# Performance work log

Measured on AMD Instinct MI355X. Metric: run time of the kernel, lower is better.

## Reference

```python
import jax, jax.numpy as jnp
import numpy as np

ROPE_BASE = 100.0  # CroCo/InfiniteVGGT-style 2D RoPE base

def _rope_1d(sub, pos, base=ROPE_BASE):
    # sub: (B,H,N,half), pos: (B,N) float
    half = sub.shape[-1]
    quarter = half // 2
    inv_freq = 1.0 / (base ** (jnp.arange(quarter, dtype=jnp.float32) / quarter))
    ang = pos[:, None, :, None] * inv_freq  # (B,1,N,quarter)
    cos, sin = jnp.cos(ang), jnp.sin(ang)
    x1, x2 = sub[..., :quarter], sub[..., quarter:]
    return jnp.concatenate([x1 * cos - x2 * sin, x1 * sin + x2 * cos], axis=-1)

def rope_2d(t, positions):
    # t: (B,H,N,Dh); positions: (B,N,2) int (y,x)
    Dh = t.shape[-1]
    half = Dh // 2
    pos_f = positions.astype(t.dtype)
    y = _rope_1d(t[..., :half], pos_f[..., 0])
    x = _rope_1d(t[..., half:], pos_f[..., 1])
    return jnp.concatenate([y, x], axis=-1)

def setup_inputs() -> dict:
    key = jax.random.key(0)
    k1, k2, k3, k4 = jax.random.split(key, 4)
    B, N, C, H = 2, 2048, 1024, 16
    x = jax.random.normal(k1, (B, N, C), dtype=jnp.float32)
    positions = jax.random.randint(k2, (B, N, 2), 0, 64, dtype=jnp.int32)
    qkv_w = jax.random.normal(k3, (3 * C, C), dtype=jnp.float32) * (C ** -0.5)
    proj_w = jax.random.normal(k4, (C, C), dtype=jnp.float32) * (C ** -0.5)
    proj_b = jnp.zeros((C,), dtype=jnp.float32)
    return {"x": x, "positions": positions, "qkv_w": qkv_w, "proj_w": proj_w, "proj_b": proj_b}

def reference(x, positions, qkv_w, proj_w, proj_b):
    B, N, C = x.shape
    H = 16
    Dh = C // H
    scale = Dh ** -0.5
    qkv = (x @ qkv_w.T).reshape(B, N, 3, H, Dh).transpose(2, 0, 3, 1, 4)  # (3,B,H,N,Dh)
    q, k, v = qkv[0], qkv[1], qkv[2]
    q = rope_2d(q, positions)
    k = rope_2d(k, positions)
    attn = jnp.einsum('bhnd,bhmd->bhnm', q, k) * scale  # (B,H,N,N)
    attn = jax.nn.softmax(attn, axis=-1)
    out = jnp.einsum('bhnm,bhmd->bhnd', attn, v)  # (B,H,N,Dh)
    out = out.transpose(0, 2, 1, 3).reshape(B, N, C)
    return out @ proj_w.T + proj_b
```

## Files before the change

kernel.cpp:

```cpp
#include <hip/hip_runtime.h>
#include <cmath>

typedef unsigned short u16;
typedef unsigned int   u32;
typedef __attribute__((ext_vector_type(8))) __bf16 bf16x8;
typedef __attribute__((ext_vector_type(2))) __bf16 bf16x2;
typedef __attribute__((ext_vector_type(4))) float  f32x4;

constexpr int BB = 2, SEQ = 2048, CH = 1024, NH = 16, DH = 64;

__device__ inline u16 f2bf(float f) {
    u32 u = __builtin_bit_cast(u32, f);
    u += 0x7FFF + ((u >> 16) & 1);
    return (u16)(u >> 16);
}
__device__ inline float bf2f(u16 b) { return __builtin_bit_cast(float, (u32)b << 16); }
__device__ inline u32 pkbf(float a, float b) {
#if __has_builtin(__builtin_amdgcn_cvt_pk_bf16_f32)
    bf16x2 r = __builtin_amdgcn_cvt_pk_bf16_f32(a, b);
    return __builtin_bit_cast(u32, r);
#else
    return (u32)f2bf(a) | ((u32)f2bf(b) << 16);
#endif
}
__device__ inline float fexp2(float x) {
#if __has_builtin(__builtin_amdgcn_exp2f)
    return __builtin_amdgcn_exp2f(x);
#else
    return exp2f(x);
#endif
}

__device__ inline void gld_lds16(const void* g, void* l) {
    __builtin_amdgcn_global_load_lds((const __attribute__((address_space(1))) void*)g,
                                     (__attribute__((address_space(3))) void*)l, 16, 0, 0);
}
__device__ inline f32x4 mfma16(bf16x8 a, bf16x8 b, f32x4 c) {
    return __builtin_amdgcn_mfma_f32_16x16x32_bf16(a, b, c, 0, 0, 0);
}
__device__ inline bf16x8 ld_frag(const u16* p) {
    return __builtin_bit_cast(bf16x8, *(const uint4*)p);
}

__global__ __launch_bounds__(256) void convert_kernel(const float* __restrict__ x,
                                                      const float* __restrict__ wq,
                                                      const float* __restrict__ wp,
                                                      u16* __restrict__ xb,
                                                      u16* __restrict__ wqb,
                                                      u16* __restrict__ wpb) {
    const int q = blockIdx.x * 256 + threadIdx.x;
    const float* src; u16* dst; int idx;
    if (q < 1048576)            { src = x;  dst = xb;  idx = q; }
    else if (q < 1048576+786432){ src = wq; dst = wqb; idx = q - 1048576; }
    else                        { src = wp; dst = wpb; idx = q - 1048576 - 786432; }
    float4 v = *(const float4*)(src + (size_t)idx * 4);
    ushort4 o; o.x = f2bf(v.x); o.y = f2bf(v.y); o.z = f2bf(v.z); o.w = f2bf(v.w);
    *(ushort4*)(dst + (size_t)idx * 4) = o;
}

__global__ __launch_bounds__(256) void gemm_qkv_rope(const u16* __restrict__ A,
                                                     const u16* __restrict__ Bw,
                                                     const int* __restrict__ pos,
                                                     u16* __restrict__ Qb,
                                                     u16* __restrict__ Kb,
                                                     u16* __restrict__ Vt) {
    __shared__ u16 smem[18432];
    u16* As = smem;
    u16* Bs = smem + 4096;
    const int t = threadIdx.x, lane = t & 63, w = t >> 6;
    const int l15 = lane & 15, quad = lane >> 4;
    const int wm = w >> 1, wn = w & 1;
    const int m0 = blockIdx.y * 128, n0 = blockIdx.x * 128;
    const int K = CH, N = 3 * CH;

    const int row0 = t >> 2, v0 = t & 3;
    const int gi0 = (v0 - (row0 >> 1)) & 3;
    const int row1 = row0 + 64;
    const int gi1 = (v0 - (row1 >> 1)) & 3;

    f32x4 acc[4][4] = {};
    for (int k0 = 0; k0 < K; k0 += 32) {
        __syncthreads();
        gld_lds16(A  + (size_t)(m0 + row0) * K + k0 + gi0 * 8, As + t * 8);
        gld_lds16(A  + (size_t)(m0 + row1) * K + k0 + gi1 * 8, As + 2048 + t * 8);
        gld_lds16(Bw + (size_t)(n0 + row0) * K + k0 + gi0 * 8, Bs + t * 8);
        gld_lds16(Bw + (size_t)(n0 + row1) * K + k0 + gi1 * 8, Bs + 2048 + t * 8);
        __syncthreads();
        bf16x8 af[4], bfv[4];
#pragma unroll
        for (int mi = 0; mi < 4; ++mi) {
            const int r = wm * 64 + mi * 16 + l15;
            af[mi] = ld_frag(As + (r * 4 + ((quad + (r >> 1)) & 3)) * 8);
        }
#pragma unroll
        for (int nj = 0; nj < 4; ++nj) {
            const int r = wn * 64 + nj * 16 + l15;
            bfv[nj] = ld_frag(Bs + (r * 4 + ((quad + (r >> 1)) & 3)) * 8);
        }
#pragma unroll
        for (int mi = 0; mi < 4; ++mi)
#pragma unroll
            for (int nj = 0; nj < 4; ++nj)
                acc[mi][nj] = mfma16(af[mi], bfv[nj], acc[mi][nj]);
    }

    const int reg = n0 >> 10;
    const int h   = ((n0 & 1023) >> 6) + wn;
    if (reg < 2) {
        const float fr = exp2f(-(float)l15 * 0.41524101186092f);
        const float scale = reg ? 1.0f : 0.18033688011112042f;
        u16* dst = reg ? Kb : Qb;
#pragma unroll
        for (int mi = 0; mi < 4; ++mi) {
#pragma unroll
            for (int r = 0; r < 4; ++r) {
                const int m = m0 + wm * 64 + mi * 16 + quad * 4 + r;
                const int bh = (m >> 11) * NH + h;
                const int n  = m & 2047;
                float sy, cy, sx, cx;
                sincosf((float)pos[m * 2]     * fr, &sy, &cy);
                sincosf((float)pos[m * 2 + 1] * fr, &sx, &cx);
                cy *= scale; sy *= scale; cx *= scale; sx *= scale;
                const float x1 = acc[mi][0][r], x2 = acc[mi][1][r];
                const float y1 = acc[mi][2][r], y2 = acc[mi][3][r];
                u16* p = dst + ((size_t)bh * SEQ + n) * 64 + l15;
                p[0]  = f2bf(x1 * cy - x2 * sy);
                p[16] = f2bf(x1 * sy + x2 * cy);
                p[32] = f2bf(y1 * cx - y2 * sx);
                p[48] = f2bf(y1 * sx + y2 * cx);
            }
        }
    } else {
        __syncthreads();
        u16* T = smem + w * 4608;
#pragma unroll
        for (int mi = 0; mi < 4; ++mi)
#pragma unroll
            for (int nj = 0; nj < 4; ++nj)
#pragma unroll
                for (int r = 0; r < 4; ++r)
                    T[(nj * 16 + l15) * 72 + mi * 16 + quad * 4 + r] =
                        f2bf(acc[mi][nj][r]);
        const int bh = (m0 >> 11) * NH + h;
        const int nbase = (m0 & 2047) + wm * 64;
        u16* gdst = Vt + ((size_t)bh * 64 + lane) * SEQ + nbase;
#pragma unroll
        for (int j = 0; j < 8; ++j)
            *(uint4*)(gdst + j * 8) = *(const uint4*)(T + lane * 72 + j * 8);
    }
}

__global__ __launch_bounds__(256) void gemm_bf16(const u16* __restrict__ A,
                                                 const u16* __restrict__ Bw,
                                                 const float* __restrict__ bias,
                                                 float* __restrict__ C,
                                                 int M, int N, int K) {
    __shared__ u16 As[128 * 32];
    __shared__ u16 Bs[128 * 32];
    const int t = threadIdx.x, lane = t & 63, w = t >> 6;
    const int l15 = lane & 15, quad = lane >> 4;
    const int wm = w >> 1, wn = w & 1;
    const int m0 = blockIdx.y * 128, n0 = blockIdx.x * 128;

    const int row0 = t >> 2, v0 = t & 3;
    const int gi0 = (v0 - (row0 >> 1)) & 3;
    const int row1 = row0 + 64;
    const int gi1 = (v0 - (row1 >> 1)) & 3;

    f32x4 acc[4][4] = {};
    for (int k0 = 0; k0 < K; k0 += 32) {
        __syncthreads();
        gld_lds16(A  + (size_t)(m0 + row0) * K + k0 + gi0 * 8, As + t * 8);
        gld_lds16(A  + (size_t)(m0 + row1) * K + k0 + gi1 * 8, As + 2048 + t * 8);
        gld_lds16(Bw + (size_t)(n0 + row0) * K + k0 + gi0 * 8, Bs + t * 8);
        gld_lds16(Bw + (size_t)(n0 + row1) * K + k0 + gi1 * 8, Bs + 2048 + t * 8);
        __syncthreads();
        bf16x8 af[4], bfv[4];
#pragma unroll
        for (int mi = 0; mi < 4; ++mi) {
            const int r = wm * 64 + mi * 16 + l15;
            af[mi] = ld_frag(As + (r * 4 + ((quad + (r >> 1)) & 3)) * 8);
        }
#pragma unroll
        for (int nj = 0; nj < 4; ++nj) {
            const int r = wn * 64 + nj * 16 + l15;
            bfv[nj] = ld_frag(Bs + (r * 4 + ((quad + (r >> 1)) & 3)) * 8);
        }
#pragma unroll
        for (int mi = 0; mi < 4; ++mi)
#pragma unroll
            for (int nj = 0; nj < 4; ++nj)
                acc[mi][nj] = mfma16(af[mi], bfv[nj], acc[mi][nj]);
    }
#pragma unroll
    for (int mi = 0; mi < 4; ++mi)
#pragma unroll
        for (int nj = 0; nj < 4; ++nj) {
            const int n = n0 + wn * 64 + nj * 16 + l15;
            const float bv = bias[n];
#pragma unroll
            for (int r = 0; r < 4; ++r) {
                const int m = m0 + wm * 64 + mi * 16 + quad * 4 + r;
                C[(size_t)m * N + n] = acc[mi][nj][r] + bv;
            }
        }
}

__global__ __launch_bounds__(256, 4) void attn_mfma(const u16* __restrict__ Qb,
                                                    const u16* __restrict__ Kb,
                                                    const u16* __restrict__ Vt,
                                                    u16* __restrict__ Opart,
                                                    float* __restrict__ lpart) {
    __shared__ u16 Ks[64 * 64];
    __shared__ u16 Vs[64 * 64];
    __shared__ u16 Ps[128 * 72];
    const int t = threadIdx.x, lane = t & 63, w = t >> 6;
    const int l15 = lane & 15, quad = lane >> 4;
    const int bh = blockIdx.y;
    const int q0 = blockIdx.x * 128;
    const int z  = blockIdx.z;

    const int rowA = t >> 3, vA = t & 7;
    const int giA = (vA - rowA) & 7;
    const int rowB = rowA + 32;
    const int giB = (vA - rowB) & 7;

    const size_t kbase = (size_t)bh * SEQ * 64;
    const size_t vbase = (size_t)bh * 64 * SEQ;

    const uint4 ones_u = {0x3F803F80u, 0x3F803F80u, 0x3F803F80u, 0x3F803F80u};
    const bf16x8 onesf = __builtin_bit_cast(bf16x8, ones_u);

    bf16x8 aq[2][2];
#pragma unroll
    for (int mi = 0; mi < 2; ++mi)
#pragma unroll
        for (int ks = 0; ks < 2; ++ks)
            aq[mi][ks] = ld_frag(Qb + ((size_t)bh * SEQ + q0 + w * 32 + mi * 16 + l15) * 64
                                 + ks * 32 + quad * 8);

    f32x4 oacc[2][4] = {};
    f32x4 lacc[2] = {};

    for (int kt = 0; kt < 16; ++kt) {
        const int k0 = z * 1024 + kt * 64;
        __syncthreads();
        gld_lds16(Kb + kbase + (size_t)(k0 + rowA) * 64 + giA * 8, Ks + t * 8);
        gld_lds16(Kb + kbase + (size_t)(k0 + rowB) * 64 + giB * 8, Ks + 2048 + t * 8);
        gld_lds16(Vt + vbase + (size_t)rowA * SEQ + k0 + giA * 8, Vs + t * 8);
        gld_lds16(Vt + vbase + (size_t)rowB * SEQ + k0 + giB * 8, Vs + 2048 + t * 8);
        __syncthreads();

        f32x4 sacc[2][4] = {};
#pragma unroll
        for (int ks = 0; ks < 2; ++ks)
#pragma unroll
            for (int nk = 0; nk < 4; ++nk) {
                const int rK = nk * 16 + l15;
                const bf16x8 kf = ld_frag(Ks + (rK * 8 + (((ks * 4 + quad) + rK) & 7)) * 8);
                sacc[0][nk] = mfma16(kf, aq[0][ks], sacc[0][nk]);
                sacc[1][nk] = mfma16(kf, aq[1][ks], sacc[1][nk]);
            }

#pragma unroll
        for (int mi = 0; mi < 2; ++mi) {
            const int prow = (w * 32 + mi * 16 + l15) * 72;
#pragma unroll
            for (int nk = 0; nk < 4; ++nk) {
                const float p0 = fexp2(sacc[mi][nk][0]);
                const float p1 = fexp2(sacc[mi][nk][1]);
                const float p2 = fexp2(sacc[mi][nk][2]);
                const float p3 = fexp2(sacc[mi][nk][3]);
                uint2 pk; pk.x = pkbf(p0, p1); pk.y = pkbf(p2, p3);
                *(uint2*)&Ps[prow + nk * 16 + quad * 4] = pk;
            }
        }

#pragma unroll
        for (int ks = 0; ks < 2; ++ks) {
            const bf16x8 ap0 = ld_frag(Ps + (w * 32 + l15) * 72 + ks * 32 + quad * 8);
            const bf16x8 ap1 = ld_frag(Ps + (w * 32 + 16 + l15) * 72 + ks * 32 + quad * 8);
            lacc[0] = mfma16(ap0, onesf, lacc[0]);
            lacc[1] = mfma16(ap1, onesf, lacc[1]);
#pragma unroll
            for (int nj = 0; nj < 4; ++nj) {
                const int rV = nj * 16 + l15;
                const bf16x8 vf = ld_frag(Vs + (rV * 8 + (((ks * 4 + quad) + rV) & 7)) * 8);
                oacc[0][nj] = mfma16(ap0, vf, oacc[0][nj]);
                oacc[1][nj] = mfma16(ap1, vf, oacc[1][nj]);
            }
        }
    }

#pragma unroll
    for (int mi = 0; mi < 2; ++mi)
#pragma unroll
        for (int r = 0; r < 4; ++r) {
            const int qrow = q0 + w * 32 + mi * 16 + quad * 4 + r;
            if (l15 == 0)
                lpart[((size_t)z * 32 + bh) * SEQ + qrow] = lacc[mi][r];
            const size_t orow = (((size_t)z * 32 + bh) * SEQ + qrow) * 64;
#pragma unroll
            for (int nj = 0; nj < 4; ++nj)
                Opart[orow + nj * 16 + l15] = f2bf(oacc[mi][nj][r]);
        }
}

__global__ __launch_bounds__(256) void merge_kernel(const u16* __restrict__ Opart,
                                                    const float* __restrict__ lpart,
                                                    u16* __restrict__ Ob) {
    const int gid = blockIdx.x * 256 + threadIdx.x;
    const int d4 = gid & 15, q = (gid >> 4) & 2047, bh = gid >> 15;
    const size_t i1 = ((size_t)bh * SEQ + q) * 64 + d4 * 4;
    const size_t i2 = i1 + (size_t)32 * SEQ * 64;
    const float inv = 1.0f / (lpart[(size_t)bh * SEQ + q] +
                              lpart[(size_t)(32 + bh) * SEQ + q]);
    const ushort4 a = *(const ushort4*)(Opart + i1);
    const ushort4 b = *(const ushort4*)(Opart + i2);
    ushort4 o;
    o.x = f2bf((bf2f(a.x) + bf2f(b.x)) * inv);
    o.y = f2bf((bf2f(a.y) + bf2f(b.y)) * inv);
    o.z = f2bf((bf2f(a.z) + bf2f(b.z)) * inv);
    o.w = f2bf((bf2f(a.w) + bf2f(b.w)) * inv);
    const int b_ = bh >> 4, h = bh & 15;
    *(ushort4*)(Ob + ((size_t)(b_ * SEQ + q)) * CH + h * 64 + d4 * 4) = o;
}

extern "C" void kernel_launch(void* const* d_in, const int* in_sizes, int n_in,
                              void* d_out, int out_size, void* d_ws, size_t ws_size,
                              hipStream_t stream) {
    const float* x      = (const float*)d_in[0];
    const int*   pos    = (const int*)d_in[1];
    const float* qkv_w  = (const float*)d_in[2];
    const float* proj_w = (const float*)d_in[3];
    const float* proj_b = (const float*)d_in[4];
    float* out = (float*)d_out;

    u16* ws = (u16*)d_ws;
    u16* x_bf    = ws;
    u16* attn_bf = ws;
    u16* wq_bf   = ws + 4194304;
    float* lpart = (float*)(ws + 4194304);
    u16* wp_bf   = ws + 7340032;
    u16* Qb      = ws + 8388608;
    u16* Kb      = ws + 12582912;
    u16* Vt      = ws + 16777216;
    u16* Opart   = ws + 20971520;

    const int M = BB * SEQ;

    convert_kernel<<<8192, 256, 0, stream>>>(x, qkv_w, proj_w, x_bf, wq_bf, wp_bf);
    gemm_qkv_rope<<<dim3(3 * CH / 128, M / 128), 256, 0, stream>>>(
        x_bf, wq_bf, pos, Qb, Kb, Vt);
    attn_mfma<<<dim3(SEQ / 128, BB * NH, 2), 256, 0, stream>>>(Qb, Kb, Vt, Opart, lpart);
    merge_kernel<<<4096, 256, 0, stream>>>(Opart, lpart, attn_bf);
    gemm_bf16<<<dim3(CH / 128, M / 128), 256, 0, stream>>>(
        attn_bf, wp_bf, proj_b, out, M, CH, CH);
}
```

Measured before the change: 218.3 us.

## Double-buffer LDS in both GEMMs and precompute RoPE sin/cos table

Both GEMM kernels now prefetch the next K-tile into a second LDS buffer while computing on the current one, cutting one barrier per iteration and overlapping global loads with MFMA. The convert kernel additionally builds a small cos/sin table (with the Q scale folded in) so the QKV epilogue does table lookups instead of sincosf. The table assumes positions are below 64 and is placed in a workspace region later reused by attention partials.

```diff
diff --git a/kernel.cpp b/kernel.cpp
--- a/kernel.cpp
+++ b/kernel.cpp
@@ -47,8 +47,23 @@
                                                       const float* __restrict__ wp,
                                                       u16* __restrict__ xb,
                                                       u16* __restrict__ wqb,
-                                                      u16* __restrict__ wpb) {
+                                                      u16* __restrict__ wpb,
+                                                      float2* __restrict__ tabq,
+                                                      float2* __restrict__ tabk) {
     const int q = blockIdx.x * 256 + threadIdx.x;
+    if (q >= 2097152) {
+        const int idx = q - 2097152;
+        if (idx < 1024) {
+            const int p = idx >> 4, i = idx & 15;
+            const float f = exp2f(-(float)i * 0.41524101186092f);
+            float s, c;
+            sincosf((float)p * f, &s, &c);
+            tabk[idx] = make_float2(c, s);
+            tabq[idx] = make_float2(c * 0.18033688011112042f,
+                                    s * 0.18033688011112042f);
+        }
+        return;
+    }
     const float* src; u16* dst; int idx;
     if (q < 1048576)            { src = x;  dst = xb;  idx = q; }
     else if (q < 1048576+786432){ src = wq; dst = wqb; idx = q - 1048576; }
@@ -61,41 +76,57 @@
 __global__ __launch_bounds__(256) void gemm_qkv_rope(const u16* __restrict__ A,
                                                      const u16* __restrict__ Bw,
                                                      const int* __restrict__ pos,
+                                                     const float2* __restrict__ tabq,
+                                                     const float2* __restrict__ tabk,
                                                      u16* __restrict__ Qb,
                                                      u16* __restrict__ Kb,
                                                      u16* __restrict__ Vt) {
     __shared__ u16 smem[18432];
-    u16* As = smem;
-    u16* Bs = smem + 4096;
     const int t = threadIdx.x, lane = t & 63, w = t >> 6;
     const int l15 = lane & 15, quad = lane >> 4;
     const int wm = w >> 1, wn = w & 1;
     const int m0 = blockIdx.y * 128, n0 = blockIdx.x * 128;
-    const int K = CH, N = 3 * CH;
+    const int K = CH;
 
     const int row0 = t >> 2, v0 = t & 3;
     const int gi0 = (v0 - (row0 >> 1)) & 3;
     const int row1 = row0 + 64;
     const int gi1 = (v0 - (row1 >> 1)) & 3;
 
+    const u16* A0 = A  + (size_t)(m0 + row0) * K + gi0 * 8;
+    const u16* A1 = A  + (size_t)(m0 + row1) * K + gi1 * 8;
+    const u16* B0 = Bw + (size_t)(n0 + row0) * K + gi0 * 8;
+    const u16* B1 = Bw + (size_t)(n0 + row1) * K + gi1 * 8;
+
+    gld_lds16(A0, smem + t * 8);
+    gld_lds16(A1, smem + 2048 + t * 8);
+    gld_lds16(B0, smem + 8192 + t * 8);
+    gld_lds16(B1, smem + 10240 + t * 8);
+
     f32x4 acc[4][4] = {};
-    for (int k0 = 0; k0 < K; k0 += 32) {
+    for (int kt = 0; kt < K / 32; ++kt) {
         __syncthreads();
-        gld_lds16(A  + (size_t)(m0 + row0) * K + k0 + gi0 * 8, As + t * 8);
-        gld_lds16(A  + (size_t)(m0 + row1) * K + k0 + gi1 * 8, As + 2048 + t * 8);
-        gld_lds16(Bw + (size_t)(n0 + row0) * K + k0 + gi0 * 8, Bs + t * 8);
-        gld_lds16(Bw + (size_t)(n0 + row1) * K + k0 + gi1 * 8, Bs + 2048 + t * 8);
-        __syncthreads();
+        const int cur = (kt & 1) * 4096;
+        if (kt + 1 < K / 32) {
+            const int off = (kt + 1) * 32;
+            const int nxt = ((kt + 1) & 1) * 4096;
+            gld_lds16(A0 + off, smem + nxt + t * 8);
+            gld_lds16(A1 + off, smem + nxt + 2048 + t * 8);
+            gld_lds16(B0 + off, smem + 8192 + nxt + t * 8);
+            gld_lds16(B1 + off, smem + 8192 + nxt + 2048 + t * 8);
+        }
+        const u16* as = smem + cur;
+        const u16* bs = smem + 8192 + cur;
         bf16x8 af[4], bfv[4];
 #pragma unroll
         for (int mi = 0; mi < 4; ++mi) {
             const int r = wm * 64 + mi * 16 + l15;
-            af[mi] = ld_frag(As + (r * 4 + ((quad + (r >> 1)) & 3)) * 8);
+            af[mi] = ld_frag(as + (r * 4 + ((quad + (r >> 1)) & 3)) * 8);
         }
 #pragma unroll
         for (int nj = 0; nj < 4; ++nj) {
             const int r = wn * 64 + nj * 16 + l15;
-            bfv[nj] = ld_frag(Bs + (r * 4 + ((quad + (r >> 1)) & 3)) * 8);
+            bfv[nj] = ld_frag(bs + (r * 4 + ((quad + (r >> 1)) & 3)) * 8);
         }
 #pragma unroll
         for (int mi = 0; mi < 4; ++mi)
@@ -107,8 +138,7 @@
     const int reg = n0 >> 10;
     const int h   = ((n0 & 1023) >> 6) + wn;
     if (reg < 2) {
-        const float fr = exp2f(-(float)l15 * 0.41524101186092f);
-        const float scale = reg ? 1.0f : 0.18033688011112042f;
+        const float2* tab = reg ? tabk : tabq;
         u16* dst = reg ? Kb : Qb;
 #pragma unroll
         for (int mi = 0; mi < 4; ++mi) {
@@ -117,17 +147,16 @@
                 const int m = m0 + wm * 64 + mi * 16 + quad * 4 + r;
                 const int bh = (m >> 11) * NH + h;
                 const int n  = m & 2047;
-                float sy, cy, sx, cx;
-                sincosf((float)pos[m * 2]     * fr, &sy, &cy);
-                sincosf((float)pos[m * 2 + 1] * fr, &sx, &cx);
-                cy *= scale; sy *= scale; cx *= scale; sx *= scale;
+                const int2 pp = *(const int2*)(pos + m * 2);
+                const float2 ty = tab[pp.x * 16 + l15];
+                const float2 tx = tab[pp.y * 16 + l15];
                 const float x1 = acc[mi][0][r], x2 = acc[mi][1][r];
                 const float y1 = acc[mi][2][r], y2 = acc[mi][3][r];
                 u16* p = dst + ((size_t)bh * SEQ + n) * 64 + l15;
-                p[0]  = f2bf(x1 * cy - x2 * sy);
-                p[16] = f2bf(x1 * sy + x2 * cy);
-                p[32] = f2bf(y1 * cx - y2 * sx);
-                p[48] = f2bf(y1 * sx + y2 * cx);
+                p[0]  = f2bf(x1 * ty.x - x2 * ty.y);
+                p[16] = f2bf(x1 * ty.y + x2 * ty.x);
+                p[32] = f2bf(y1 * tx.x - y2 * tx.y);
+                p[48] = f2bf(y1 * tx.y + y2 * tx.x);
             }
         }
     } else {
@@ -155,8 +184,7 @@
                                                  const float* __restrict__ bias,
                                                  float* __restrict__ C,
                                                  int M, int N, int K) {
-    __shared__ u16 As[128 * 32];
-    __shared__ u16 Bs[128 * 32];
+    __shared__ u16 smem[16384];
     const int t = threadIdx.x, lane = t & 63, w = t >> 6;
     const int l15 = lane & 15, quad = lane >> 4;
     const int wm = w >> 1, wn = w & 1;
@@ -167,24 +195,40 @@
     const int row1 = row0 + 64;
     const int gi1 = (v0 - (row1 >> 1)) & 3;
 
+    const u16* A0 = A  + (size_t)(m0 + row0) * K + gi0 * 8;
+    const u16* A1 = A  + (size_t)(m0 + row1) * K + gi1 * 8;
+    const u16* B0 = Bw + (size_t)(n0 + row0) * K + gi0 * 8;
+    const u16* B1 = Bw + (size_t)(n0 + row1) * K + gi1 * 8;
+
+    gld_lds16(A0, smem + t * 8);
+    gld_lds16(A1, smem + 2048 + t * 8);
+    gld_lds16(B0, smem + 8192 + t * 8);
+    gld_lds16(B1, smem + 10240 + t * 8);
+
     f32x4 acc[4][4] = {};
-    for (int k0 = 0; k0 < K; k0 += 32) {
+    for (int kt = 0; kt < K / 32; ++kt) {
         __syncthreads();
-        gld_lds16(A  + (size_t)(m0 + row0) * K + k0 + gi0 * 8, As + t * 8);
-        gld_lds16(A  + (size_t)(m0 + row1) * K + k0 + gi1 * 8, As + 2048 + t * 8);
-        gld_lds16(Bw + (size_t)(n0 + row0) * K + k0 + gi0 * 8, Bs + t * 8);
-        gld_lds16(Bw + (size_t)(n0 + row1) * K + k0 + gi1 * 8, Bs + 2048 + t * 8);
-        __syncthreads();
+        const int cur = (kt & 1) * 4096;
+        if (kt + 1 < K / 32) {
+            const int off = (kt + 1) * 32;
+            const int nxt = ((kt + 1) & 1) * 4096;
+            gld_lds16(A0 + off, smem + nxt + t * 8);
+            gld_lds16(A1 + off, smem + nxt + 2048 + t * 8);
+            gld_lds16(B0 + off, smem + 8192 + nxt + t * 8);
+            gld_lds16(B1 + off, smem + 8192 + nxt + 2048 + t * 8);
+        }
+        const u16* as = smem + cur;
+        const u16* bs = smem + 8192 + cur;
         bf16x8 af[4], bfv[4];
 #pragma unroll
         for (int mi = 0; mi < 4; ++mi) {
             const int r = wm * 64 + mi * 16 + l15;
-            af[mi] = ld_frag(As + (r * 4 + ((quad + (r >> 1)) & 3)) * 8);
+            af[mi] = ld_frag(as + (r * 4 + ((quad + (r >> 1)) & 3)) * 8);
         }
 #pragma unroll
         for (int nj = 0; nj < 4; ++nj) {
             const int r = wn * 64 + nj * 16 + l15;
-            bfv[nj] = ld_frag(Bs + (r * 4 + ((quad + (r >> 1)) & 3)) * 8);
+            bfv[nj] = ld_frag(bs + (r * 4 + ((quad + (r >> 1)) & 3)) * 8);
         }
 #pragma unroll
         for (int mi = 0; mi < 4; ++mi)
@@ -346,12 +390,15 @@
     u16* Kb      = ws + 12582912;
     u16* Vt      = ws + 16777216;
     u16* Opart   = ws + 20971520;
+    float2* tabq = (float2*)(ws + 20971520);
+    float2* tabk = (float2*)(ws + 20971520 + 4096);
 
     const int M = BB * SEQ;
 
-    convert_kernel<<<8192, 256, 0, stream>>>(x, qkv_w, proj_w, x_bf, wq_bf, wp_bf);
+    convert_kernel<<<8196, 256, 0, stream>>>(x, qkv_w, proj_w, x_bf, wq_bf, wp_bf,
+                                             tabq, tabk);
     gemm_qkv_rope<<<dim3(3 * CH / 128, M / 128), 256, 0, stream>>>(
-        x_bf, wq_bf, pos, Qb, Kb, Vt);
+        x_bf, wq_bf, pos, tabq, tabk, Qb, Kb, Vt);
     attn_mfma<<<dim3(SEQ / 128, BB * NH, 2), 256, 0, stream>>>(Qb, Kb, Vt, Opart, lpart);
     merge_kernel<<<4096, 256, 0, stream>>>(Opart, lpart, attn_bf);
     gemm_bf16<<<dim3(CH / 128, M / 128), 256, 0, stream>>>(
```

Result: faster. 201.6 us (-7.7%).
